# Kernel tuning notes

Measured on AMD Instinct MI355X. Metric: run time of the kernel, lower is better.

## Reference

```python
import jax, jax.numpy as jnp
import numpy as np

D_MODEL = 1024
NUM_HEADS = 16
HEAD_DIM = D_MODEL // NUM_HEADS


def setup_inputs() -> dict:
    key = jax.random.key(0)
    kx, kq, kk, kv, ko = jax.random.split(key, 5)
    B, S = 2, 2048
    scale = 1.0 / np.sqrt(D_MODEL)
    return {
        "x": jax.random.normal(kx, (B, S, D_MODEL), dtype=jnp.float32),
        "W_q": jax.random.normal(kq, (D_MODEL, D_MODEL), dtype=jnp.float32) * scale,
        "W_k": jax.random.normal(kk, (D_MODEL, D_MODEL), dtype=jnp.float32) * scale,
        "W_v": jax.random.normal(kv, (D_MODEL, D_MODEL), dtype=jnp.float32) * scale,
        "W_o": jax.random.normal(ko, (D_MODEL, D_MODEL), dtype=jnp.float32) * scale,
        "causal": 1,
    }


def _attn(x, W_q, W_k, W_v, W_o, causal):
    B, S, D = x.shape
    H, Hd = NUM_HEADS, HEAD_DIM
    # projections: nn.Linear applies x @ W.T
    q = (x @ W_q.T).reshape(B, S, H, Hd)
    k = (x @ W_k.T).reshape(B, S, H, Hd)
    v = (x @ W_v.T).reshape(B, S, H, Hd)
    # scores: [B, H, S, S]
    scores = jnp.einsum("bqhd,bkhd->bhqk", q, k) / np.sqrt(Hd)
    if causal:
        mask = jnp.triu(jnp.ones((S, S), dtype=bool), k=1)
        scores = jnp.where(mask, -jnp.inf, scores)
    attn = jax.nn.softmax(scores, axis=-1)
    out = jnp.einsum("bhqk,bkhd->bqhd", attn, v).reshape(B, S, D)
    return out @ W_o.T


def reference(x, W_q, W_k, W_v, W_o, causal):
    return _attn(x, W_q, W_k, W_v, W_o, causal)
```

## Files before the change

### kernel.cpp

```cpp
#include <hip/hip_runtime.h>

typedef __attribute__((ext_vector_type(8))) short bf16x8;
typedef __attribute__((ext_vector_type(4))) float f32x4;
typedef __attribute__((ext_vector_type(4))) unsigned short u16x4;

#define MFMA16(a, b, c) __builtin_amdgcn_mfma_f32_16x16x32_bf16((a), (b), (c), 0, 0, 0)

static constexpr int D_MODEL = 1024;
static constexpr int SEQ = 2048;
static constexpr int NH = 16;
static constexpr int HD = 64;
static constexpr int LDA = 40;
static constexpr int MST = 136;
static constexpr float NEG_BIG = -1.0e30f;

__device__ __forceinline__ unsigned short f2bf(float f) {
  union { float f; unsigned int u; } v; v.f = f;
  unsigned int r = v.u + 0x7fffu + ((v.u >> 16) & 1u);
  return (unsigned short)(r >> 16);
}

__device__ __forceinline__ unsigned int cvtpk_bf16(float a, float b) {
  unsigned int r;
  asm("v_cvt_pk_bf16_f32 %0, %1, %2" : "=v"(r) : "v"(a), "v"(b));
  return r;
}

__device__ __forceinline__ bf16x8 ld8(const void* p, size_t eidx, int bf) {
  if (bf) return *(const bf16x8*)((const unsigned short*)p + eidx);
  const float* f = (const float*)p + eidx;
  f32x4 lo = *(const f32x4*)f;
  f32x4 hi = *(const f32x4*)(f + 4);
  bf16x8 r;
  r[0] = (short)f2bf(lo[0]); r[1] = (short)f2bf(lo[1]);
  r[2] = (short)f2bf(lo[2]); r[3] = (short)f2bf(lo[3]);
  r[4] = (short)f2bf(hi[0]); r[5] = (short)f2bf(hi[1]);
  r[6] = (short)f2bf(hi[2]); r[7] = (short)f2bf(hi[3]);
  return r;
}

__device__ __forceinline__ void async16(const unsigned short* g, unsigned short* l) {
  __builtin_amdgcn_global_load_lds(
      (const __attribute__((address_space(1))) void*)g,
      (__attribute__((address_space(3))) void*)l, 16, 0, 0);
}

__global__ __launch_bounds__(64) void detect_kernel(
    const unsigned short* __restrict__ xs, int* __restrict__ flag) {
  int lane = threadIdx.x;
  unsigned short s = xs[2 * lane];
  int e = (s >> 7) & 0xFF;
  bool hit = (e >= 117 && e <= 129);
  unsigned long long m = __ballot(hit);
  if (lane == 0) { flag[0] = (__popcll(m) >= 32) ? 1 : 0; flag[1] = 1; }
}

__global__ __launch_bounds__(256) void convert_kernel(
    const void* __restrict__ X,
    const void* __restrict__ W0, const void* __restrict__ W1,
    const void* __restrict__ W2, const void* __restrict__ W3,
    const int* __restrict__ flag,
    unsigned short* __restrict__ Xb, unsigned short* __restrict__ Wb)
{
  const int bf = *flag;
  const int ty = blockIdx.y;
  const void* src; unsigned short* dst; size_t n;
  if (ty == 0) { src = X; dst = Xb; n = (size_t)2 * SEQ * D_MODEL; }
  else {
    src = (ty == 1) ? W0 : (ty == 2) ? W1 : (ty == 3) ? W2 : W3;
    dst = Wb + (size_t)(ty - 1) * D_MODEL * D_MODEL;
    n = (size_t)D_MODEL * D_MODEL;
  }
  size_t i = ((size_t)blockIdx.x * 256 + threadIdx.x) * 8;
  if (i >= n) return;
  *(bf16x8*)(dst + i) = ld8(src, i, bf);
}

__device__ __forceinline__ void gemm_fast_core(
    const unsigned short* __restrict__ A, const unsigned short* __restrict__ B,
    int tm, int tn, unsigned short* smem, f32x4 acc[4][4])
{
  const int t = threadIdx.x;
  const int lane = t & 63;
  const int w = t >> 6;
  const int wm = (w >> 1) * 64, wn = (w & 1) * 64;
  const int quad = lane >> 4, l16 = lane & 15;
  const int srow = lane >> 2;
  const int scol = ((lane & 3) ^ ((lane >> 3) & 3)) * 8;
  const int xa = (l16 >> 1) & 3;

#pragma unroll
  for (int mi = 0; mi < 4; ++mi)
#pragma unroll
    for (int ni = 0; ni < 4; ++ni)
      acc[mi][ni] = (f32x4){0.f, 0.f, 0.f, 0.f};

  auto stage = [&](int f, int buf) {
    const int k0 = f * 32;
    unsigned short* dst = smem + buf * 8192;
#pragma unroll
    for (int i = 0; i < 2; ++i) {
      const int row = w * 32 + i * 16;
      async16(A + (size_t)(tm + row + srow) * D_MODEL + k0 + scol,
              dst + row * 32);
      async16(B + (size_t)(tn + row + srow) * D_MODEL + k0 + scol,
              dst + 4096 + row * 32);
    }
  };

  stage(0, 0);
  stage(1, 1);

  int cur = 0, nb = 2;
  for (int f = 0; f < 32; ++f) {
    if (f + 1 < 32) asm volatile("s_waitcnt vmcnt(4)" ::: "memory");
    else            asm volatile("s_waitcnt vmcnt(0)" ::: "memory");
    __builtin_amdgcn_s_barrier();
    __builtin_amdgcn_sched_barrier(0);
    if (f + 2 < 32) stage(f + 2, nb);
    const unsigned short* As = smem + cur * 8192;
    const unsigned short* Bs = As + 4096;
    bf16x8 af[4], bfv[4];
#pragma unroll
    for (int mi = 0; mi < 4; ++mi)
      af[mi] = *(const bf16x8*)(As + (wm + mi * 16 + l16) * 32 + (quad ^ xa) * 8);
#pragma unroll
    for (int ni = 0; ni < 4; ++ni)
      bfv[ni] = *(const bf16x8*)(Bs + (wn + ni * 16 + l16) * 32 + (quad ^ xa) * 8);
    __builtin_amdgcn_s_setprio(1);
#pragma unroll
    for (int mi = 0; mi < 4; ++mi)
#pragma unroll
      for (int ni = 0; ni < 4; ++ni)
        acc[mi][ni] = MFMA16(af[mi], bfv[ni], acc[mi][ni]);
    __builtin_amdgcn_s_setprio(0);
    cur = (cur == 2) ? 0 : cur + 1;
    nb = (nb == 2) ? 0 : nb + 1;
  }
}

__global__ __launch_bounds__(256) void qkv_fast_kernel(
    const unsigned short* __restrict__ X,
    const unsigned short* __restrict__ Wb,
    unsigned short* __restrict__ qd,
    unsigned short* __restrict__ kws,
    unsigned short* __restrict__ vws)
{
  __shared__ __align__(16) unsigned short smem[3 * 8192];
  const int bid = blockIdx.x;
  const int xcd = bid & 7, s0 = bid >> 3;
  const int tmg = xcd >> 2, tng = xcd & 3;
  const int tm_local = s0 / 6, zt = s0 % 6;
  const int z = zt >> 1, tn_local = zt & 1;
  const int tm = (tmg * 16 + tm_local) * 128;
  const int tn = (tng * 2 + tn_local) * 128;
  const unsigned short* W = Wb + (size_t)z * D_MODEL * D_MODEL;
  f32x4 acc[4][4];
  gemm_fast_core(X, W, tm, tn, smem, acc);

  const int t = threadIdx.x;
  const int lane = t & 63, w = t >> 6;
  const int wm = (w >> 1) * 64, wn = (w & 1) * 64;
  const int quad = lane >> 4, l16 = lane & 15;

  if (z == 2) {
    const int b = tm >> 11;
    const int sb = tm & 2047;
#pragma unroll
    for (int ph = 0; ph < 2; ++ph) {
      __syncthreads();
      if ((w & 1) == ph) {
#pragma unroll
        for (int mi = 0; mi < 4; ++mi)
#pragma unroll
          for (int ni = 0; ni < 4; ++ni)
#pragma unroll
            for (int r = 0; r < 4; ++r) {
              int m_local = wm + mi * 16 + quad * 4 + r;
              int n_sub = ni * 16 + l16;
              smem[n_sub * MST + m_local] = f2bf(acc[mi][ni][r]);
            }
      }
      __syncthreads();
      const int row = t >> 2, c0 = (t & 3) * 32;
      const int n_g = tn + ph * 64 + row;
      const int h = n_g >> 6, d = n_g & 63;
      unsigned short* dst = vws + (((size_t)b * NH + h) * HD + d) * SEQ + sb + c0;
#pragma unroll
      for (int cc = 0; cc < 4; ++cc)
        *(bf16x8*)(dst + cc * 8) = *(const bf16x8*)(smem + row * MST + c0 + cc * 8);
    }
    return;
  }
#pragma unroll
  for (int mi = 0; mi < 4; ++mi)
#pragma unroll
    for (int ni = 0; ni < 4; ++ni)
#pragma unroll
      for (int r = 0; r < 4; ++r) {
        int m = tm + wm + mi * 16 + quad * 4 + r;
        int n = tn + wn + ni * 16 + l16;
        unsigned short bv = f2bf(acc[mi][ni][r]);
        if (z == 0) {
          qd[(size_t)m * D_MODEL + n] = bv;
        } else {
          int b = m >> 11, sg = m & 2047;
          int h = n >> 6, d = n & 63;
          kws[(((size_t)b * NH + h) * SEQ + sg) * HD + d] = bv;
        }
      }
}

__global__ __launch_bounds__(256) void oproj_fast_kernel(
    const unsigned short* __restrict__ AW,
    const unsigned short* __restrict__ Wo,
    float* __restrict__ tmp)
{
  __shared__ __align__(16) unsigned short smem[3 * 8192];
  const int bid = blockIdx.x;
  const int xcd = bid & 7, s0 = bid >> 3;
  const int tmg = xcd >> 2, tng = xcd & 3;
  const int tm = (tmg * 16 + (s0 >> 1)) * 128;
  const int tn = (tng * 2 + (s0 & 1)) * 128;
  f32x4 acc[4][4];
  gemm_fast_core(AW, Wo, tm, tn, smem, acc);

  const int t = threadIdx.x;
  const int lane = t & 63, w = t >> 6;
  const int wm = (w >> 1) * 64, wn = (w & 1) * 64;
  const int quad = lane >> 4, l16 = lane & 15;
#pragma unroll
  for (int mi = 0; mi < 4; ++mi)
#pragma unroll
    for (int ni = 0; ni < 4; ++ni)
#pragma unroll
      for (int r = 0; r < 4; ++r) {
        int m = tm + wm + mi * 16 + quad * 4 + r;
        int n = tn + wn + ni * 16 + l16;
        tmp[(size_t)m * D_MODEL + n] = acc[mi][ni][r];
      }
}

__device__ __forceinline__ void gemm_tile_128x128(
    const void* __restrict__ A, const void* __restrict__ B, int bf,
    int tm, int tn, unsigned short* As, unsigned short* Bs, f32x4 acc[4][4])
{
  const int t = threadIdx.x;
  const int lane = t & 63;
  const int w = t >> 6;
  const int wm = (w >> 1) * 64, wn = (w & 1) * 64;
  const int quad = lane >> 4, l16 = lane & 15;
  const int r0 = t >> 2, kc = (t & 3) * 8;
  const int r1 = r0 + 64;

#pragma unroll
  for (int mi = 0; mi < 4; ++mi)
#pragma unroll
    for (int ni = 0; ni < 4; ++ni)
      acc[mi][ni] = (f32x4){0.f, 0.f, 0.f, 0.f};

  for (int k0 = 0; k0 < D_MODEL; k0 += 32) {
    bf16x8 a0 = ld8(A, (size_t)(tm + r0) * D_MODEL + k0 + kc, bf);
    bf16x8 a1 = ld8(A, (size_t)(tm + r1) * D_MODEL + k0 + kc, bf);
    bf16x8 b0 = ld8(B, (size_t)(tn + r0) * D_MODEL + k0 + kc, bf);
    bf16x8 b1 = ld8(B, (size_t)(tn + r1) * D_MODEL + k0 + kc, bf);
    __syncthreads();
    *(bf16x8*)(As + r0 * LDA + kc) = a0;
    *(bf16x8*)(As + r1 * LDA + kc) = a1;
    *(bf16x8*)(Bs + r0 * LDA + kc) = b0;
    *(bf16x8*)(Bs + r1 * LDA + kc) = b1;
    __syncthreads();
    bf16x8 af[4], bfv[4];
#pragma unroll
    for (int mi = 0; mi < 4; ++mi)
      af[mi] = *(const bf16x8*)(As + (wm + mi * 16 + l16) * LDA + quad * 8);
#pragma unroll
    for (int ni = 0; ni < 4; ++ni)
      bfv[ni] = *(const bf16x8*)(Bs + (wn + ni * 16 + l16) * LDA + quad * 8);
#pragma unroll
    for (int mi = 0; mi < 4; ++mi)
#pragma unroll
      for (int ni = 0; ni < 4; ++ni)
        acc[mi][ni] = MFMA16(af[mi], bfv[ni], acc[mi][ni]);
  }
}

__global__ __launch_bounds__(256) void qkv_kernel(
    const void* __restrict__ X,
    const void* __restrict__ Wq,
    const void* __restrict__ Wk,
    const void* __restrict__ Wv,
    const int* __restrict__ flag,
    unsigned short* __restrict__ qd,
    unsigned short* __restrict__ kws,
    unsigned short* __restrict__ vws)
{
  __shared__ __align__(16) unsigned short As[128 * LDA];
  __shared__ __align__(16) unsigned short Bs[128 * LDA];
  const int bf = *flag;
  const int z = blockIdx.z;
  const void* W = (z == 0) ? Wq : ((z == 1) ? Wk : Wv);
  const int tm = blockIdx.y * 128, tn = blockIdx.x * 128;
  f32x4 acc[4][4];
  gemm_tile_128x128(X, W, bf, tm, tn, As, Bs, acc);

  const int t = threadIdx.x;
  const int lane = t & 63, w = t >> 6;
  const int wm = (w >> 1) * 64, wn = (w & 1) * 64;
  const int quad = lane >> 4, l16 = lane & 15;
#pragma unroll
  for (int mi = 0; mi < 4; ++mi)
#pragma unroll
    for (int ni = 0; ni < 4; ++ni)
#pragma unroll
      for (int r = 0; r < 4; ++r) {
        int m = tm + wm + mi * 16 + quad * 4 + r;
        int n = tn + wn + ni * 16 + l16;
        unsigned short bv = f2bf(acc[mi][ni][r]);
        if (z == 0) {
          qd[(size_t)m * D_MODEL + n] = bv;
        } else {
          int b = m >> 11, s = m & 2047;
          int h = n >> 6, d = n & 63;
          if (z == 1) kws[(((size_t)b * NH + h) * SEQ + s) * HD + d] = bv;
          else        vws[(((size_t)b * NH + h) * HD + d) * SEQ + s] = bv;
        }
      }
}

__global__ __launch_bounds__(256) void oproj_kernel(
    const unsigned short* __restrict__ AW,
    const void* __restrict__ Wo,
    const int* __restrict__ flag,
    float* __restrict__ tmp)
{
  __shared__ __align__(16) unsigned short As[128 * LDA];
  __shared__ __align__(16) unsigned short Bs[128 * LDA];
  const int bf = *flag;
  const int t = threadIdx.x;
  const int lane = t & 63;
  const int w = t >> 6;
  const int wm = (w >> 1) * 64, wn = (w & 1) * 64;
  const int quad = lane >> 4, l16 = lane & 15;
  const int r0 = t >> 2, kc = (t & 3) * 8;
  const int r1 = r0 + 64;
  const int tm = blockIdx.y * 128, tn = blockIdx.x * 128;
  f32x4 acc[4][4];
#pragma unroll
  for (int mi = 0; mi < 4; ++mi)
#pragma unroll
    for (int ni = 0; ni < 4; ++ni)
      acc[mi][ni] = (f32x4){0.f, 0.f, 0.f, 0.f};

  for (int k0 = 0; k0 < D_MODEL; k0 += 32) {
    bf16x8 a0 = *(const bf16x8*)(AW + (size_t)(tm + r0) * D_MODEL + k0 + kc);
    bf16x8 a1 = *(const bf16x8*)(AW + (size_t)(tm + r1) * D_MODEL + k0 + kc);
    bf16x8 b0 = ld8(Wo, (size_t)(tn + r0) * D_MODEL + k0 + kc, bf);
    bf16x8 b1 = ld8(Wo, (size_t)(tn + r1) * D_MODEL + k0 + kc, bf);
    __syncthreads();
    *(bf16x8*)(As + r0 * LDA + kc) = a0;
    *(bf16x8*)(As + r1 * LDA + kc) = a1;
    *(bf16x8*)(Bs + r0 * LDA + kc) = b0;
    *(bf16x8*)(Bs + r1 * LDA + kc) = b1;
    __syncthreads();
    bf16x8 af[4], bfv[4];
#pragma unroll
    for (int mi = 0; mi < 4; ++mi)
      af[mi] = *(const bf16x8*)(As + (wm + mi * 16 + l16) * LDA + quad * 8);
#pragma unroll
    for (int ni = 0; ni < 4; ++ni)
      bfv[ni] = *(const bf16x8*)(Bs + (wn + ni * 16 + l16) * LDA + quad * 8);
#pragma unroll
    for (int mi = 0; mi < 4; ++mi)
#pragma unroll
      for (int ni = 0; ni < 4; ++ni)
        acc[mi][ni] = MFMA16(af[mi], bfv[ni], acc[mi][ni]);
  }
#pragma unroll
  for (int mi = 0; mi < 4; ++mi)
#pragma unroll
    for (int ni = 0; ni < 4; ++ni)
#pragma unroll
      for (int r = 0; r < 4; ++r) {
        int m = tm + wm + mi * 16 + quad * 4 + r;
        int n = tn + wn + ni * 16 + l16;
        tmp[(size_t)m * D_MODEL + n] = acc[mi][ni][r];
      }
}

__device__ __forceinline__ void attn_item(
    const unsigned short* __restrict__ Ksb, const unsigned short* __restrict__ Vsb,
    const bf16x8 (&aq)[2][2], f32x4 (&oaccT)[2][4], float (&lsum)[2],
    int kt, int diag, int q0base, int l16, int quad, int xa, float Cs)
{
  bf16x8 kfr[4][2], vfr[4][2];
#pragma unroll
  for (int cb = 0; cb < 4; ++cb)
#pragma unroll
    for (int hf = 0; hf < 2; ++hf) {
      kfr[cb][hf] = *(const bf16x8*)(Ksb + (cb * 16 + l16) * 64 +
                                     ((hf * 4 + quad) ^ xa) * 8);
      vfr[cb][hf] = *(const bf16x8*)(Vsb + (cb * 16 + l16) * 64 +
                                     ((hf * 4 + quad) ^ xa) * 8);
    }
#pragma unroll
  for (int s = 0; s < 2; ++s) {
    f32x4 sc[4];
    __builtin_amdgcn_s_setprio(1);
#pragma unroll
    for (int cb = 0; cb < 4; ++cb) {
      sc[cb] = (f32x4){0.f, 0.f, 0.f, 0.f};
      sc[cb] = MFMA16(kfr[cb][0], aq[s][0], sc[cb]);
      sc[cb] = MFMA16(kfr[cb][1], aq[s][1], sc[cb]);
    }
    __builtin_amdgcn_s_setprio(0);
    if (diag) {
      int qq = q0base + s * 16 + l16;
#pragma unroll
      for (int cb = 0; cb < 4; ++cb)
#pragma unroll
        for (int rr = 0; rr < 4; ++rr)
          if (kt * 64 + (cb & 1) * 32 + quad * 8 + (cb >> 1) * 4 + rr > qq)
            sc[cb][rr] = NEG_BIG;
    }
    float ls = 0.f;
#pragma unroll
    for (int cb = 0; cb < 4; ++cb)
#pragma unroll
      for (int rr = 0; rr < 4; ++rr) {
        float pv = __builtin_amdgcn_exp2f(sc[cb][rr] * Cs);
        ls += pv;
        sc[cb][rr] = pv;
      }
    lsum[s] += ls;
    bf16x8 bp[2];
#pragma unroll
    for (int hf = 0; hf < 2; ++hf) {
      union { unsigned int w4[4]; bf16x8 v; } u;
      u.w4[0] = cvtpk_bf16(sc[hf][0], sc[hf][1]);
      u.w4[1] = cvtpk_bf16(sc[hf][2], sc[hf][3]);
      u.w4[2] = cvtpk_bf16(sc[2 + hf][0], sc[2 + hf][1]);
      u.w4[3] = cvtpk_bf16(sc[2 + hf][2], sc[2 + hf][3]);
      bp[hf] = u.v;
    }
    __builtin_amdgcn_s_setprio(1);
#pragma unroll
    for (int db = 0; db < 4; ++db) {
      oaccT[s][db] = MFMA16(vfr[db][0], bp[0], oaccT[s][db]);
      oaccT[s][db] = MFMA16(vfr[db][1], bp[1], oaccT[s][db]);
    }
    __builtin_amdgcn_s_setprio(0);
  }
}

__global__ __launch_bounds__(128, 1) void attn_kernel(
    unsigned short* __restrict__ Qd,
    const unsigned short* __restrict__ Kb,
    const unsigned short* __restrict__ Vt,
    const int* __restrict__ causal_p)
{
  __shared__ __align__(16) unsigned short Ks[3][64 * 64];
  __shared__ __align__(16) unsigned short Vs[3][64 * 64];
  const int bid = blockIdx.x;
  const int xcd = bid & 7, slot = bid >> 3;
  const int bhl = slot >> 4, p = slot & 15;
  const int bh = xcd * 4 + bhl;
  const int b = bh >> 4, h = bh & 15;
  const int t = threadIdx.x, lane = t & 63, w = t >> 6;
  const int quad = lane >> 4, l16 = lane & 15;
  const int causal = *causal_p;
  const int tA = causal ? (31 - p) : (2 * p);
  const int tB = causal ? p : (2 * p + 1);
  const int ktA = causal ? (32 - p) : 32;
  const int ITEMS = causal ? 33 : 64;
  unsigned short* qh = Qd + (size_t)b * SEQ * D_MODEL + h * HD;
  const unsigned short* kh = Kb + ((size_t)b * NH + h) * SEQ * HD;
  const unsigned short* vh = Vt + ((size_t)b * NH + h) * HD * SEQ;
  const float Cs = 0.125f * 1.4426950408889634f;
  const int srow = lane >> 3;
  const int gcol = ((lane & 7) ^ srow) * 8;
  const int xa = l16 & 7;

  int kvp[4];
#pragma unroll
  for (int j2 = 0; j2 < 4; ++j2) {
    const int rp = w * 32 + j2 * 8 + srow;
    kvp[j2] = ((rp >> 4) & 1) * 32 + ((rp >> 2) & 3) * 8 + ((rp >> 5) & 1) * 4 + (rp & 3);
  }

  const int qA = tA * 64 + w * 32, qB = tB * 64 + w * 32;
  bf16x8 aqA[2][2], aqB[2][2];
#pragma unroll
  for (int s = 0; s < 2; ++s)
#pragma unroll
    for (int ch = 0; ch < 2; ++ch) {
      aqA[s][ch] = *(const bf16x8*)(qh + (size_t)(qA + s * 16 + l16) * D_MODEL +
                                    ch * 32 + quad * 8);
      aqB[s][ch] = *(const bf16x8*)(qh + (size_t)(qB + s * 16 + l16) * D_MODEL +
                                    ch * 32 + quad * 8);
    }

  f32x4 oaccA[2][4], oaccB[2][4];
#pragma unroll
  for (int s = 0; s < 2; ++s)
#pragma unroll
    for (int db = 0; db < 4; ++db) {
      oaccA[s][db] = (f32x4){0.f, 0.f, 0.f, 0.f};
      oaccB[s][db] = (f32x4){0.f, 0.f, 0.f, 0.f};
    }
  float lsumA[2] = {0.f, 0.f}, lsumB[2] = {0.f, 0.f};

  auto stage = [&](int f, int buf) {
    const int kt = (f < ktA) ? f : (f - ktA);
#pragma unroll
    for (int j2 = 0; j2 < 4; ++j2) {
      const int row = w * 32 + j2 * 8;
      async16(kh + (size_t)(kt * 64 + kvp[j2]) * HD + gcol, &Ks[buf][row * 64]);
      async16(vh + (size_t)(row + srow) * SEQ + kt * 64 + gcol, &Vs[buf][row * 64]);
    }
  };

  stage(0, 0);
  stage(1, 1);

  int cur = 0, nb = 2;
  for (int f = 0; f < ITEMS; ++f) {
    if (f + 1 < ITEMS) asm volatile("s_waitcnt vmcnt(8)" ::: "memory");
    else               asm volatile("s_waitcnt vmcnt(0)" ::: "memory");
    __builtin_amdgcn_s_barrier();
    __builtin_amdgcn_sched_barrier(0);
    if (f + 2 < ITEMS) stage(f + 2, nb);
    if (f < ktA)
      attn_item(&Ks[cur][0], &Vs[cur][0], aqA, oaccA, lsumA,
                f, causal && (f == ktA - 1), qA, l16, quad, xa, Cs);
    else
      attn_item(&Ks[cur][0], &Vs[cur][0], aqB, oaccB, lsumB,
                f - ktA, causal && (f == ITEMS - 1), qB, l16, quad, xa, Cs);
    cur = (cur == 2) ? 0 : cur + 1;
    nb = (nb == 2) ? 0 : nb + 1;
  }

#pragma unroll
  for (int s = 0; s < 2; ++s) {
    float l = lsumA[s];
    l += __shfl_xor(l, 16, 64);
    l += __shfl_xor(l, 32, 64);
    float inv = 1.0f / l;
#pragma unroll
    for (int db = 0; db < 4; ++db) {
      u16x4 o;
#pragma unroll
      for (int rr = 0; rr < 4; ++rr) o[rr] = f2bf(oaccA[s][db][rr] * inv);
      *(u16x4*)(qh + (size_t)(qA + s * 16 + l16) * D_MODEL + db * 16 + quad * 4) = o;
    }
  }
#pragma unroll
  for (int s = 0; s < 2; ++s) {
    float l = lsumB[s];
    l += __shfl_xor(l, 16, 64);
    l += __shfl_xor(l, 32, 64);
    float inv = 1.0f / l;
#pragma unroll
    for (int db = 0; db < 4; ++db) {
      u16x4 o;
#pragma unroll
      for (int rr = 0; rr < 4; ++rr) o[rr] = f2bf(oaccB[s][db][rr] * inv);
      *(u16x4*)(qh + (size_t)(qB + s * 16 + l16) * D_MODEL + db * 16 + quad * 4) = o;
    }
  }
}

__global__ __launch_bounds__(256) void final_kernel(
    const float* __restrict__ tmp, void* __restrict__ out,
    const int* __restrict__ flag)
{
  const int bf = *flag;
  size_t i = ((size_t)blockIdx.x * 256 + threadIdx.x) * 8;
  f32x4 lo = *(const f32x4*)(tmp + i);
  f32x4 hi = *(const f32x4*)(tmp + i + 4);
  if (bf) {
    bf16x8 r;
    r[0] = (short)f2bf(lo[0]); r[1] = (short)f2bf(lo[1]);
    r[2] = (short)f2bf(lo[2]); r[3] = (short)f2bf(lo[3]);
    r[4] = (short)f2bf(hi[0]); r[5] = (short)f2bf(hi[1]);
    r[6] = (short)f2bf(hi[2]); r[7] = (short)f2bf(hi[3]);
    *(bf16x8*)((unsigned short*)out + i) = r;
  } else {
    *(f32x4*)((float*)out + i) = lo;
    *(f32x4*)((float*)out + i + 4) = hi;
  }
}

extern "C" void kernel_launch(void* const* d_in, const int* in_sizes, int n_in,
                              void* d_out, int out_size, void* d_ws, size_t ws_size,
                              hipStream_t stream) {
  const void* X  = d_in[0];
  const void* Wq = d_in[1];
  const void* Wk = d_in[2];
  const void* Wv = d_in[3];
  const void* Wo = d_in[4];
  const int* causal = (const int*)d_in[5];

  const size_t NE = (size_t)2 * SEQ * D_MODEL;
  const size_t WE = (size_t)D_MODEL * D_MODEL;
  int* flag0 = (int*)d_ws;
  unsigned short* kws = (unsigned short*)((char*)d_ws + 64);
  unsigned short* vws = kws + NE;
  float* tmp = (float*)kws;
  unsigned short* Wb = vws + NE;
  unsigned short* qd = (unsigned short*)d_out;
  unsigned short* Xb = qd + NE;

  const bool big = ws_size >= (size_t)64 + 24ull * 1024 * 1024;

  hipLaunchKernelGGL(detect_kernel, dim3(1), dim3(64), 0, stream,
                     (const unsigned short*)X, flag0);
  if (big) {
    hipLaunchKernelGGL(convert_kernel, dim3(2048, 5), dim3(256), 0, stream,
                       X, Wq, Wk, Wv, Wo, flag0, Xb, Wb);
    hipLaunchKernelGGL(qkv_fast_kernel, dim3(768), dim3(256), 0, stream,
                       Xb, Wb, qd, kws, vws);
    hipLaunchKernelGGL(attn_kernel, dim3(512), dim3(128), 0, stream,
                       qd, kws, vws, causal);
    hipLaunchKernelGGL(oproj_fast_kernel, dim3(256), dim3(256), 0, stream,
                       qd, Wb + 3 * WE, tmp);
  } else {
    hipLaunchKernelGGL(qkv_kernel, dim3(8, 32, 3), dim3(256), 0, stream,
                       X, Wq, Wk, Wv, flag0, qd, kws, vws);
    hipLaunchKernelGGL(attn_kernel, dim3(512), dim3(128), 0, stream,
                       qd, kws, vws, causal);
    hipLaunchKernelGGL(oproj_kernel, dim3(8, 32), dim3(256), 0, stream,
                       qd, Wo, flag0, tmp);
  }
  hipLaunchKernelGGL(final_kernel, dim3(2048), dim3(256), 0, stream,
                     tmp, d_out, flag0);
}
```

Measured before the change: 194.6 us.

## Split attention block across four waves with 16 query rows each

The attention kernel goes from 2 waves of 128 threads, each handling 32 query rows (two 16-row sub-tiles), to 4 waves of 256 threads, each handling 16 rows. K/V staging is spread over four waves, so each issues half as many async loads and the vmcnt wait drops from 8 to 4. Launch bounds become (256,2) to allow more waves per CU and hide latency. In exchange, each K/V fragment load from LDS is reused by half as many MFMAs, and register pressure is capped at two blocks per CU. The row-sum reduction is also reordered into a tree of adds.

```diff
diff --git a/kernel.cpp b/kernel.cpp
--- a/kernel.cpp
+++ b/kernel.cpp
@@ -390,7 +390,7 @@
 
 __device__ __forceinline__ void attn_item(
     const unsigned short* __restrict__ Ksb, const unsigned short* __restrict__ Vsb,
-    const bf16x8 (&aq)[2][2], f32x4 (&oaccT)[2][4], float (&lsum)[2],
+    const bf16x8 (&aq)[2], f32x4 (&oacc)[4], float& lsum,
     int kt, int diag, int q0base, int l16, int quad, int xa, float Cs)
 {
   bf16x8 kfr[4][2], vfr[4][2];
@@ -403,57 +403,57 @@
       vfr[cb][hf] = *(const bf16x8*)(Vsb + (cb * 16 + l16) * 64 +
                                      ((hf * 4 + quad) ^ xa) * 8);
     }
-#pragma unroll
-  for (int s = 0; s < 2; ++s) {
-    f32x4 sc[4];
-    __builtin_amdgcn_s_setprio(1);
-#pragma unroll
-    for (int cb = 0; cb < 4; ++cb) {
-      sc[cb] = (f32x4){0.f, 0.f, 0.f, 0.f};
-      sc[cb] = MFMA16(kfr[cb][0], aq[s][0], sc[cb]);
-      sc[cb] = MFMA16(kfr[cb][1], aq[s][1], sc[cb]);
-    }
-    __builtin_amdgcn_s_setprio(0);
-    if (diag) {
-      int qq = q0base + s * 16 + l16;
-#pragma unroll
-      for (int cb = 0; cb < 4; ++cb)
-#pragma unroll
-        for (int rr = 0; rr < 4; ++rr)
-          if (kt * 64 + (cb & 1) * 32 + quad * 8 + (cb >> 1) * 4 + rr > qq)
-            sc[cb][rr] = NEG_BIG;
-    }
-    float ls = 0.f;
+  f32x4 sc[4];
+  __builtin_amdgcn_s_setprio(1);
+#pragma unroll
+  for (int cb = 0; cb < 4; ++cb) {
+    sc[cb] = (f32x4){0.f, 0.f, 0.f, 0.f};
+    sc[cb] = MFMA16(kfr[cb][0], aq[0], sc[cb]);
+    sc[cb] = MFMA16(kfr[cb][1], aq[1], sc[cb]);
+  }
+  __builtin_amdgcn_s_setprio(0);
+  if (diag) {
+    int qq = q0base + l16;
 #pragma unroll
     for (int cb = 0; cb < 4; ++cb)
 #pragma unroll
-      for (int rr = 0; rr < 4; ++rr) {
-        float pv = __builtin_amdgcn_exp2f(sc[cb][rr] * Cs);
-        ls += pv;
-        sc[cb][rr] = pv;
-      }
-    lsum[s] += ls;
-    bf16x8 bp[2];
-#pragma unroll
-    for (int hf = 0; hf < 2; ++hf) {
-      union { unsigned int w4[4]; bf16x8 v; } u;
-      u.w4[0] = cvtpk_bf16(sc[hf][0], sc[hf][1]);
-      u.w4[1] = cvtpk_bf16(sc[hf][2], sc[hf][3]);
-      u.w4[2] = cvtpk_bf16(sc[2 + hf][0], sc[2 + hf][1]);
-      u.w4[3] = cvtpk_bf16(sc[2 + hf][2], sc[2 + hf][3]);
-      bp[hf] = u.v;
-    }
-    __builtin_amdgcn_s_setprio(1);
-#pragma unroll
-    for (int db = 0; db < 4; ++db) {
-      oaccT[s][db] = MFMA16(vfr[db][0], bp[0], oaccT[s][db]);
-      oaccT[s][db] = MFMA16(vfr[db][1], bp[1], oaccT[s][db]);
-    }
-    __builtin_amdgcn_s_setprio(0);
-  }
-}
-
-__global__ __launch_bounds__(128, 1) void attn_kernel(
+      for (int rr = 0; rr < 4; ++rr)
+        if (kt * 64 + (cb & 1) * 32 + quad * 8 + (cb >> 1) * 4 + rr > qq)
+          sc[cb][rr] = NEG_BIG;
+  }
+#pragma unroll
+  for (int cb = 0; cb < 4; ++cb)
+#pragma unroll
+    for (int rr = 0; rr < 4; ++rr)
+      sc[cb][rr] = __builtin_amdgcn_exp2f(sc[cb][rr] * Cs);
+  f32x4 t0, t1;
+#pragma unroll
+  for (int rr = 0; rr < 4; ++rr) { t0[rr] = sc[0][rr] + sc[1][rr]; }
+#pragma unroll
+  for (int rr = 0; rr < 4; ++rr) { t1[rr] = sc[2][rr] + sc[3][rr]; }
+#pragma unroll
+  for (int rr = 0; rr < 4; ++rr) { t0[rr] += t1[rr]; }
+  lsum += (t0[0] + t0[1]) + (t0[2] + t0[3]);
+  bf16x8 bp[2];
+#pragma unroll
+  for (int hf = 0; hf < 2; ++hf) {
+    union { unsigned int w4[4]; bf16x8 v; } u;
+    u.w4[0] = cvtpk_bf16(sc[hf][0], sc[hf][1]);
+    u.w4[1] = cvtpk_bf16(sc[hf][2], sc[hf][3]);
+    u.w4[2] = cvtpk_bf16(sc[2 + hf][0], sc[2 + hf][1]);
+    u.w4[3] = cvtpk_bf16(sc[2 + hf][2], sc[2 + hf][3]);
+    bp[hf] = u.v;
+  }
+  __builtin_amdgcn_s_setprio(1);
+#pragma unroll
+  for (int db = 0; db < 4; ++db) {
+    oacc[db] = MFMA16(vfr[db][0], bp[0], oacc[db]);
+    oacc[db] = MFMA16(vfr[db][1], bp[1], oacc[db]);
+  }
+  __builtin_amdgcn_s_setprio(0);
+}
+
+__global__ __launch_bounds__(256, 2) void attn_kernel(
     unsigned short* __restrict__ Qd,
     const unsigned short* __restrict__ Kb,
     const unsigned short* __restrict__ Vt,
@@ -481,40 +481,36 @@
   const int gcol = ((lane & 7) ^ srow) * 8;
   const int xa = l16 & 7;
 
-  int kvp[4];
-#pragma unroll
-  for (int j2 = 0; j2 < 4; ++j2) {
-    const int rp = w * 32 + j2 * 8 + srow;
+  int kvp[2];
+#pragma unroll
+  for (int j2 = 0; j2 < 2; ++j2) {
+    const int rp = w * 16 + j2 * 8 + srow;
     kvp[j2] = ((rp >> 4) & 1) * 32 + ((rp >> 2) & 3) * 8 + ((rp >> 5) & 1) * 4 + (rp & 3);
   }
 
-  const int qA = tA * 64 + w * 32, qB = tB * 64 + w * 32;
-  bf16x8 aqA[2][2], aqB[2][2];
-#pragma unroll
-  for (int s = 0; s < 2; ++s)
-#pragma unroll
-    for (int ch = 0; ch < 2; ++ch) {
-      aqA[s][ch] = *(const bf16x8*)(qh + (size_t)(qA + s * 16 + l16) * D_MODEL +
-                                    ch * 32 + quad * 8);
-      aqB[s][ch] = *(const bf16x8*)(qh + (size_t)(qB + s * 16 + l16) * D_MODEL +
-                                    ch * 32 + quad * 8);
-    }
-
-  f32x4 oaccA[2][4], oaccB[2][4];
-#pragma unroll
-  for (int s = 0; s < 2; ++s)
-#pragma unroll
-    for (int db = 0; db < 4; ++db) {
-      oaccA[s][db] = (f32x4){0.f, 0.f, 0.f, 0.f};
-      oaccB[s][db] = (f32x4){0.f, 0.f, 0.f, 0.f};
-    }
-  float lsumA[2] = {0.f, 0.f}, lsumB[2] = {0.f, 0.f};
+  const int qA = tA * 64 + w * 16, qB = tB * 64 + w * 16;
+  bf16x8 aqA[2], aqB[2];
+#pragma unroll
+  for (int ch = 0; ch < 2; ++ch) {
+    aqA[ch] = *(const bf16x8*)(qh + (size_t)(qA + l16) * D_MODEL +
+                               ch * 32 + quad * 8);
+    aqB[ch] = *(const bf16x8*)(qh + (size_t)(qB + l16) * D_MODEL +
+                               ch * 32 + quad * 8);
+  }
+
+  f32x4 oaccA[4], oaccB[4];
+#pragma unroll
+  for (int db = 0; db < 4; ++db) {
+    oaccA[db] = (f32x4){0.f, 0.f, 0.f, 0.f};
+    oaccB[db] = (f32x4){0.f, 0.f, 0.f, 0.f};
+  }
+  float lsumA = 0.f, lsumB = 0.f;
 
   auto stage = [&](int f, int buf) {
     const int kt = (f < ktA) ? f : (f - ktA);
 #pragma unroll
-    for (int j2 = 0; j2 < 4; ++j2) {
-      const int row = w * 32 + j2 * 8;
+    for (int j2 = 0; j2 < 2; ++j2) {
+      const int row = w * 16 + j2 * 8;
       async16(kh + (size_t)(kt * 64 + kvp[j2]) * HD + gcol, &Ks[buf][row * 64]);
       async16(vh + (size_t)(row + srow) * SEQ + kt * 64 + gcol, &Vs[buf][row * 64]);
     }
@@ -525,7 +521,7 @@
 
   int cur = 0, nb = 2;
   for (int f = 0; f < ITEMS; ++f) {
-    if (f + 1 < ITEMS) asm volatile("s_waitcnt vmcnt(8)" ::: "memory");
+    if (f + 1 < ITEMS) asm volatile("s_waitcnt vmcnt(4)" ::: "memory");
     else               asm volatile("s_waitcnt vmcnt(0)" ::: "memory");
     __builtin_amdgcn_s_barrier();
     __builtin_amdgcn_sched_barrier(0);
@@ -540,9 +536,8 @@
     nb = (nb == 2) ? 0 : nb + 1;
   }
 
-#pragma unroll
-  for (int s = 0; s < 2; ++s) {
-    float l = lsumA[s];
+  {
+    float l = lsumA;
     l += __shfl_xor(l, 16, 64);
     l += __shfl_xor(l, 32, 64);
     float inv = 1.0f / l;
@@ -550,13 +545,12 @@
     for (int db = 0; db < 4; ++db) {
       u16x4 o;
 #pragma unroll
-      for (int rr = 0; rr < 4; ++rr) o[rr] = f2bf(oaccA[s][db][rr] * inv);
-      *(u16x4*)(qh + (size_t)(qA + s * 16 + l16) * D_MODEL + db * 16 + quad * 4) = o;
+      for (int rr = 0; rr < 4; ++rr) o[rr] = f2bf(oaccA[db][rr] * inv);
+      *(u16x4*)(qh + (size_t)(qA + l16) * D_MODEL + db * 16 + quad * 4) = o;
     }
   }
-#pragma unroll
-  for (int s = 0; s < 2; ++s) {
-    float l = lsumB[s];
+  {
+    float l = lsumB;
     l += __shfl_xor(l, 16, 64);
     l += __shfl_xor(l, 32, 64);
     float inv = 1.0f / l;
@@ -564,8 +558,8 @@
     for (int db = 0; db < 4; ++db) {
       u16x4 o;
 #pragma unroll
-      for (int rr = 0; rr < 4; ++rr) o[rr] = f2bf(oaccB[s][db][rr] * inv);
-      *(u16x4*)(qh + (size_t)(qB + s * 16 + l16) * D_MODEL + db * 16 + quad * 4) = o;
+      for (int rr = 0; rr < 4; ++rr) o[rr] = f2bf(oaccB[db][rr] * inv);
+      *(u16x4*)(qh + (size_t)(qB + l16) * D_MODEL + db * 16 + quad * 4) = o;
     }
   }
 }
@@ -620,14 +614,14 @@
                        X, Wq, Wk, Wv, Wo, flag0, Xb, Wb);
     hipLaunchKernelGGL(qkv_fast_kernel, dim3(768), dim3(256), 0, stream,
                        Xb, Wb, qd, kws, vws);
-    hipLaunchKernelGGL(attn_kernel, dim3(512), dim3(128), 0, stream,
+    hipLaunchKernelGGL(attn_kernel, dim3(512), dim3(256), 0, stream,
                        qd, kws, vws, causal);
     hipLaunchKernelGGL(oproj_fast_kernel, dim3(256), dim3(256), 0, stream,
                        qd, Wb + 3 * WE, tmp);
   } else {
     hipLaunchKernelGGL(qkv_kernel, dim3(8, 32, 3), dim3(256), 0, stream,
                        X, Wq, Wk, Wv, flag0, qd, kws, vws);
-    hipLaunchKernelGGL(attn_kernel, dim3(512), dim3(128), 0, stream,
+    hipLaunchKernelGGL(attn_kernel, dim3(512), dim3(256), 0, stream,
                        qd, kws, vws, causal);
     hipLaunchKernelGGL(oproj_kernel, dim3(8, 32), dim3(256), 0, stream,
                        qd, Wo, flag0, tmp);
```

Result: faster. 184.0 us (-5.4%).
